# Performance work log

Hardware: AMD Instinct MI355X
Metric: run time of the kernel (lower is better)

Reference implementation:

```python
import jax, jax.numpy as jnp
import numpy as np

N_NODES = 100000
N_EDGES = 1600000
IN_CH = 165


def setup_inputs() -> dict:
    key = jax.random.key(0)
    ks = jax.random.split(key, 6)
    x = jax.random.normal(ks[0], (N_NODES, IN_CH), dtype=jnp.float32)
    edge_index = jax.random.randint(ks[1], (2, N_EDGES), 0, N_NODES, dtype=jnp.int32)
    # Glorot-ish init for weights
    W1 = jax.random.normal(ks[2], (IN_CH, 128), dtype=jnp.float32) * (1.0 / np.sqrt(IN_CH))
    b1 = jnp.zeros((128,), dtype=jnp.float32)
    W2 = jax.random.normal(ks[3], (128, 64), dtype=jnp.float32) * (1.0 / np.sqrt(128))
    b2 = jnp.zeros((64,), dtype=jnp.float32)
    Wo = jax.random.normal(ks[4], (64, 2), dtype=jnp.float32) * (1.0 / np.sqrt(64))
    bo = jnp.zeros((2,), dtype=jnp.float32)
    return {"x": x, "edge_index": edge_index, "W1": W1, "b1": b1,
            "W2": W2, "b2": b2, "Wo": Wo, "bo": bo}


def _gcn_norm(edge_index, n_nodes, dtype):
    """Add self-loops and compute symmetric normalization deg^-1/2 * deg^-1/2 (PyG gcn_norm)."""
    loops = jnp.arange(n_nodes, dtype=edge_index.dtype)
    ei = jnp.concatenate([edge_index, jnp.stack([loops, loops])], axis=1)
    row, col = ei[0], ei[1]
    deg = jax.ops.segment_sum(jnp.ones(ei.shape[1], dtype), col, num_segments=n_nodes)
    deg_inv_sqrt = jnp.where(deg > 0, jax.lax.rsqrt(deg), 0.0)
    norm = deg_inv_sqrt[row] * deg_inv_sqrt[col]  # [E+N]
    return row, col, norm


def _gcn_conv(h, row, col, norm, W, b, n_nodes):
    # transform first (F_in -> F_out), then gather-scale-scatter aggregate
    m = h @ W                                   # [N, F_out]
    msg = m[row] * norm[:, None]                # [E+N, F_out]
    agg = jax.ops.segment_sum(msg, col, num_segments=n_nodes)
    return agg + b


def reference(x, edge_index, W1, b1, W2, b2, Wo, bo):
    n_nodes = x.shape[0]
    row, col, norm = _gcn_norm(edge_index, n_nodes, x.dtype)
    h = jax.nn.relu(_gcn_conv(x, row, col, norm, W1, b1, n_nodes))
    h = jax.nn.relu(_gcn_conv(h, row, col, norm, W2, b2, n_nodes))
    return h @ Wo + bo  # [N, 2] logits
```

## Files before the change

kernel.cpp:

```cpp
#include <hip/hip_runtime.h>

#define N_NODES 100000
#define N_EDGES 1600000
#define IN_CH   165
#define SCAN_CHUNK 2048
#define NB_SCAN ((N_NODES + SCAN_CHUNK - 1) / SCAN_CHUNK)
#define BSHIFT 7
#define NBUCK  ((N_NODES + 127) / 128)
#define BCAP   3072
#define PA_BLOCKS 196

typedef unsigned short ushort_t;
typedef _Float16 f16;
typedef _Float16 f16x2 __attribute__((ext_vector_type(2)));
typedef _Float16 f16x8 __attribute__((ext_vector_type(8)));
typedef _Float16 hfrag8 __attribute__((ext_vector_type(8)));
typedef short bfrag8 __attribute__((ext_vector_type(8)));
typedef float f32x4 __attribute__((ext_vector_type(4)));

__device__ __forceinline__ ushort_t f2bf(float f) {
    unsigned u = __float_as_uint(f);
    unsigned r = (u + 0x7fffu + ((u >> 16) & 1u)) >> 16;
    return (ushort_t)r;
}
__device__ __forceinline__ float bf2f(ushort_t h) {
    return __uint_as_float(((unsigned)h) << 16);
}

__device__ __forceinline__ void fmix_lo(float& a, unsigned pair) {
    asm("v_fma_mix_f32 %0, %1, 1.0, %0 op_sel_hi:[1,0,0]" : "+v"(a) : "v"(pair));
}
__device__ __forceinline__ void fmix_hi(float& a, unsigned pair) {
    asm("v_fma_mix_f32 %0, %1, 1.0, %0 op_sel:[1,0,0] op_sel_hi:[1,0,0]" : "+v"(a) : "v"(pair));
}
__device__ __forceinline__ void fmix_acc8(float* acc, uint4 v) {
    fmix_lo(acc[0], v.x); fmix_hi(acc[1], v.x);
    fmix_lo(acc[2], v.y); fmix_hi(acc[3], v.y);
    fmix_lo(acc[4], v.z); fmix_hi(acc[5], v.z);
    fmix_lo(acc[6], v.w); fmix_hi(acc[7], v.w);
}

__global__ void scan1_kernel(const int* __restrict__ cnt, int* __restrict__ off,
                             int* __restrict__ bsum, int n) {
    __shared__ int sh[256];
    int t = threadIdx.x;
    int base = blockIdx.x * SCAN_CHUNK + t * 8;
    int v[8];
    int run = 0;
    #pragma unroll
    for (int j = 0; j < 8; ++j) {
        int c = (base + j < n) ? cnt[base + j] : 0;
        v[j] = run; run += c;
    }
    sh[t] = run;
    __syncthreads();
    for (int o = 1; o < 256; o <<= 1) {
        int x = (t >= o) ? sh[t - o] : 0;
        __syncthreads();
        sh[t] += x;
        __syncthreads();
    }
    int prev = (t > 0) ? sh[t - 1] : 0;
    #pragma unroll
    for (int j = 0; j < 8; ++j)
        if (base + j < n) off[base + j] = prev + v[j];
    if (t == 255) bsum[blockIdx.x] = sh[255];
}

__global__ void scan2_kernel(int* bsum, int nb) {
    int lane = threadIdx.x;
    int orig = (lane < nb) ? bsum[lane] : 0;
    int v = orig;
    #pragma unroll
    for (int o = 1; o < 64; o <<= 1) {
        int t = __shfl_up(v, o);
        if (lane >= o) v += t;
    }
    if (lane < nb) bsum[lane] = v - orig;
}

__global__ void scan3_kernel(int* __restrict__ off, const int* __restrict__ bsum,
                             int n, int E) {
    int i = blockIdx.x * blockDim.x + threadIdx.x;
    if (i < n) {
        off[i] = off[i] + bsum[i / SCAN_CHUNK];
    } else if (i == n) {
        off[n] = E;
    }
}

__global__ void bucketA_kernel(const int* __restrict__ row, const int* __restrict__ col,
                               int* __restrict__ bfill, unsigned* __restrict__ tmp) {
    __shared__ int lcnt[NBUCK];
    __shared__ int lcur[NBUCK];
    int t = threadIdx.x;
    int e0 = (int)((long)blockIdx.x * N_EDGES / PA_BLOCKS);
    int e1 = (int)((long)(blockIdx.x + 1) * N_EDGES / PA_BLOCKS);
    for (int i = t; i < NBUCK; i += 256) lcnt[i] = 0;
    __syncthreads();
    for (int e = e0 + t; e < e1; e += 256)
        atomicAdd(&lcnt[col[e] >> BSHIFT], 1);
    __syncthreads();
    for (int b = t; b < NBUCK; b += 256) {
        int c = lcnt[b];
        lcur[b] = (c > 0) ? (b * BCAP + atomicAdd(&bfill[b], c)) : 0;
    }
    __syncthreads();
    for (int e = e0 + t; e < e1; e += 256) {
        int cc = col[e];
        int b = cc >> BSHIFT;
        int p = atomicAdd(&lcur[b], 1);
        tmp[p] = ((unsigned)(cc & 127) << 17) | (unsigned)row[e];
    }
}

__global__ void countB_kernel(const unsigned* __restrict__ tmp, const int* __restrict__ bfill,
                              int* __restrict__ cnt, float* __restrict__ dis) {
    __shared__ int lcnt[128];
    int b = blockIdx.x, t = threadIdx.x;
    if (t < 128) lcnt[t] = 0;
    __syncthreads();
    int total = min(bfill[b], BCAP);
    const unsigned* reg = tmp + (size_t)b * BCAP;
    for (int i = t; i < total; i += 256)
        atomicAdd(&lcnt[(reg[i] >> 17) & 127], 1);
    __syncthreads();
    if (t < 128) {
        int n = (b << BSHIFT) + t;
        if (n < N_NODES) {
            int c = lcnt[t];
            cnt[n] = c;
            dis[n] = rsqrtf((float)(c + 1));
        }
    }
}

__global__ void bucketB_kernel(const unsigned* __restrict__ tmp, const int* __restrict__ bfill,
                               const int* __restrict__ off, int* __restrict__ srt) {
    __shared__ int lcur[128];
    int b = blockIdx.x;
    int t = threadIdx.x;
    int nb0 = b << BSHIFT;
    int hi = min(nb0 + 128, N_NODES);
    int base = off[nb0];
    if (t < 128) {
        int nn = nb0 + t;
        lcur[t] = (nn < hi) ? off[nn] - base : 0;
    }
    __syncthreads();
    int total = min(bfill[b], BCAP);
    const unsigned* reg = tmp + (size_t)b * BCAP;
    for (int i = t; i < total; i += 256) {
        unsigned e = reg[i];
        int c = (e >> 17) & 127;
        int r = (int)(e & 0x1FFFFu);
        int p = atomicAdd(&lcur[c], 1);
        srt[base + p] = r;
    }
}

__global__ void wsplit_kernel(const float* __restrict__ W1, const float* __restrict__ W2,
                              ushort_t* __restrict__ wt1h, ushort_t* __restrict__ wt1l,
                              ushort_t* __restrict__ wt2h, ushort_t* __restrict__ wt2l) {
    int i = blockIdx.x * 256 + threadIdx.x;
    if (i < 128 * 192) {
        int ch = i / 192, k = i - ch * 192;
        float v = (k < IN_CH) ? W1[(size_t)k * 128 + ch] : 0.f;
        ushort_t h = f2bf(v);
        wt1h[i] = h;
        wt1l[i] = f2bf(v - bf2f(h));
    } else if (i < 128 * 192 + 64 * 128) {
        int j = i - 128 * 192;
        int ch = j / 128, k = j - ch * 128;
        float v = W2[(size_t)k * 64 + ch];
        f16 h = (f16)v;
        f16 l = (f16)(v - (float)h);
        wt2h[j] = *(ushort_t*)&h;
        wt2l[j] = *(ushort_t*)&l;
    }
}

__launch_bounds__(256)
__global__ void mfma_gemm1_kernel(const float* __restrict__ X,
                                  const ushort_t* __restrict__ wth,
                                  const ushort_t* __restrict__ wtl,
                                  const float* __restrict__ dis,
                                  f16* __restrict__ M, int n_nodes) {
    constexpr int NOUT = 128, KTOT = 165, KPAD = 192;
    constexpr int NCT = NOUT / 16;
    constexpr int NCHUNK = KPAD / 32;
    constexpr int XP = 40;
    constexpr int NW = 2;
    __shared__ ushort_t xsh[64][XP];
    __shared__ ushort_t xsl[64][XP];
    __shared__ ushort_t wsh[NOUT][XP];
    __shared__ ushort_t wsl[NOUT][XP];

    int t = threadIdx.x;
    int l = t & 63, wid = t >> 6;
    long node0 = (long)blockIdx.x * 64;

    int arow = wid * 16 + (l & 15);
    int kq = (l >> 4) * 8;

    f32x4 acc[NCT];
    #pragma unroll
    for (int ct = 0; ct < NCT; ++ct) acc[ct] = (f32x4){0.f, 0.f, 0.f, 0.f};

    float xa[4], xb[4];
    bfrag8 wfh[NW], wfl[NW];

    auto loadX = [&](int c) {
        int k0 = c * 32;
        #pragma unroll
        for (int i = 0; i < 4; ++i) {
            int idx = t + i * 256;
            int node = idx >> 4, kp = idx & 15;
            long g = node0 + node;
            int k = k0 + 2 * kp;
            bool ok = (g < n_nodes);
            xa[i] = (ok && k < KTOT) ? X[g * KTOT + k] : 0.f;
            xb[i] = (ok && k + 1 < KTOT) ? X[g * KTOT + k + 1] : 0.f;
        }
    };
    auto loadW = [&](int c) {
        int k0 = c * 32;
        #pragma unroll
        for (int i = 0; i < NW; ++i) {
            int idx = t + i * 256;
            int ch = idx >> 2, q = idx & 3;
            wfh[i] = *(const bfrag8*)&wth[(size_t)ch * KPAD + k0 + q * 8];
            wfl[i] = *(const bfrag8*)&wtl[(size_t)ch * KPAD + k0 + q * 8];
        }
    };
    auto storeLDS = [&]() {
        #pragma unroll
        for (int i = 0; i < 4; ++i) {
            int idx = t + i * 256;
            int node = idx >> 4, kp = idx & 15;
            ushort_t ha = (ushort_t)(__float_as_uint(xa[i]) >> 16);
            ushort_t la = f2bf(xa[i] - bf2f(ha));
            ushort_t hb = (ushort_t)(__float_as_uint(xb[i]) >> 16);
            ushort_t lb = f2bf(xb[i] - bf2f(hb));
            *(unsigned*)&xsh[node][2 * kp] = (unsigned)ha | ((unsigned)hb << 16);
            *(unsigned*)&xsl[node][2 * kp] = (unsigned)la | ((unsigned)lb << 16);
        }
        #pragma unroll
        for (int i = 0; i < NW; ++i) {
            int idx = t + i * 256;
            int ch = idx >> 2, q = idx & 3;
            *(bfrag8*)&wsh[ch][q * 8] = wfh[i];
            *(bfrag8*)&wsl[ch][q * 8] = wfl[i];
        }
    };

    loadX(0); loadW(0);
    for (int c = 0; c < NCHUNK; ++c) {
        storeLDS();
        __syncthreads();
        if (c + 1 < NCHUNK) { loadX(c + 1); loadW(c + 1); }
        bfrag8 ah = *(const bfrag8*)&xsh[arow][kq];
        bfrag8 al = *(const bfrag8*)&xsl[arow][kq];
        #pragma unroll
        for (int ct = 0; ct < NCT; ++ct) {
            bfrag8 bh = *(const bfrag8*)&wsh[ct * 16 + (l & 15)][kq];
            bfrag8 bl = *(const bfrag8*)&wsl[ct * 16 + (l & 15)][kq];
            acc[ct] = __builtin_amdgcn_mfma_f32_16x16x32_bf16(ah, bh, acc[ct], 0, 0, 0);
            acc[ct] = __builtin_amdgcn_mfma_f32_16x16x32_bf16(ah, bl, acc[ct], 0, 0, 0);
            acc[ct] = __builtin_amdgcn_mfma_f32_16x16x32_bf16(al, bh, acc[ct], 0, 0, 0);
        }
        __syncthreads();
    }

    int nl = wid * 16 + (l >> 4) * 4;
    float dv[4];
    #pragma unroll
    for (int j = 0; j < 4; ++j) {
        long node = node0 + nl + j;
        dv[j] = (node < n_nodes) ? dis[node] : 0.f;
    }
    #pragma unroll
    for (int ct = 0; ct < NCT; ++ct) {
        int ch = ct * 16 + (l & 15);
        #pragma unroll
        for (int j = 0; j < 4; ++j) {
            long node = node0 + nl + j;
            if (node < n_nodes)
                M[node * NOUT + ch] = (f16)(acc[ct][j] * dv[j]);
        }
    }
}

__launch_bounds__(256)
__global__ void mfma_gemm2_kernel(const f16* __restrict__ X,
                                  const ushort_t* __restrict__ wth,
                                  const ushort_t* __restrict__ wtl,
                                  const float* __restrict__ dis,
                                  f16* __restrict__ M, int n_nodes) {
    constexpr int NOUT = 64, KTOT = 128;
    constexpr int NCT = NOUT / 16;
    constexpr int NCHUNK = KTOT / 32;
    constexpr int XP = 40;
    __shared__ ushort_t xs[64][XP];
    __shared__ ushort_t wsh[NOUT][XP];
    __shared__ ushort_t wsl[NOUT][XP];

    int t = threadIdx.x;
    int l = t & 63, wid = t >> 6;
    long node0 = (long)blockIdx.x * 64;

    int arow = wid * 16 + (l & 15);
    int kq = (l >> 4) * 8;

    f32x4 acc[NCT];
    #pragma unroll
    for (int ct = 0; ct < NCT; ++ct) acc[ct] = (f32x4){0.f, 0.f, 0.f, 0.f};

    unsigned xu[4];
    bfrag8 wfh, wfl;

    auto loadX = [&](int c) {
        int k0 = c * 32;
        #pragma unroll
        for (int i = 0; i < 4; ++i) {
            int idx = t + i * 256;
            int node = idx >> 4, kp = idx & 15;
            long g = node0 + node;
            xu[i] = (g < n_nodes) ? *(const unsigned*)&X[g * KTOT + k0 + 2 * kp] : 0u;
        }
    };
    auto loadW = [&](int c) {
        int k0 = c * 32;
        int ch = t >> 2, q = t & 3;
        wfh = *(const bfrag8*)&wth[(size_t)ch * KTOT + k0 + q * 8];
        wfl = *(const bfrag8*)&wtl[(size_t)ch * KTOT + k0 + q * 8];
    };
    auto storeLDS = [&]() {
        #pragma unroll
        for (int i = 0; i < 4; ++i) {
            int idx = t + i * 256;
            int node = idx >> 4, kp = idx & 15;
            *(unsigned*)&xs[node][2 * kp] = xu[i];
        }
        int ch = t >> 2, q = t & 3;
        *(bfrag8*)&wsh[ch][q * 8] = wfh;
        *(bfrag8*)&wsl[ch][q * 8] = wfl;
    };

    loadX(0); loadW(0);
    for (int c = 0; c < NCHUNK; ++c) {
        storeLDS();
        __syncthreads();
        if (c + 1 < NCHUNK) { loadX(c + 1); loadW(c + 1); }
        hfrag8 a = *(const hfrag8*)&xs[arow][kq];
        #pragma unroll
        for (int ct = 0; ct < NCT; ++ct) {
            hfrag8 bh = *(const hfrag8*)&wsh[ct * 16 + (l & 15)][kq];
            hfrag8 bl = *(const hfrag8*)&wsl[ct * 16 + (l & 15)][kq];
            acc[ct] = __builtin_amdgcn_mfma_f32_16x16x32_f16(a, bh, acc[ct], 0, 0, 0);
            acc[ct] = __builtin_amdgcn_mfma_f32_16x16x32_f16(a, bl, acc[ct], 0, 0, 0);
        }
        __syncthreads();
    }

    int nl = wid * 16 + (l >> 4) * 4;
    float dv[4];
    #pragma unroll
    for (int j = 0; j < 4; ++j) {
        long node = node0 + nl + j;
        dv[j] = (node < n_nodes) ? dis[node] : 0.f;
    }
    #pragma unroll
    for (int ct = 0; ct < NCT; ++ct) {
        int ch = ct * 16 + (l & 15);
        #pragma unroll
        for (int j = 0; j < 4; ++j) {
            long node = node0 + nl + j;
            if (node < n_nodes)
                M[node * NOUT + ch] = (f16)(acc[ct][j] * dv[j]);
        }
    }
}

__global__ void agg1_kernel(const f16* __restrict__ ms, const int* __restrict__ srt,
                            const int* __restrict__ off, const float* __restrict__ dis,
                            const float* __restrict__ b1, f16* __restrict__ h1) {
    int wave = threadIdx.x >> 6;
    int lane = threadIdx.x & 63;
    int n = blockIdx.x * 4 + wave;
    if (n >= N_NODES) return;
    int g = lane >> 4, p = lane & 15;
    const char* msb = (const char*)ms;
    unsigned pb = (unsigned)p * 16;
    float dn = dis[n];
    float acc[8] = {0.f, 0.f, 0.f, 0.f, 0.f, 0.f, 0.f, 0.f};
    if (g == 0) {
        uint4 v = *(const uint4*)(msb + (unsigned)n * 256 + pb);
        fmix_acc8(acc, v);
    }
    int s0 = off[n], s1 = off[n + 1];
    int sv = (s0 + lane < s1) ? srt[s0 + lane] : 0;
    for (int base = s0; base < s1; base += 64) {
        int nb2 = base + 64;
        int svn = (nb2 + lane < s1) ? srt[nb2 + lane] : 0;
        int cnt = min(64, s1 - base);
        int j = 0;
        for (; j + 15 < cnt; j += 16) {
            unsigned o0 = (unsigned)__shfl(sv, j + g) * 256 + pb;
            unsigned o1 = (unsigned)__shfl(sv, j + 4 + g) * 256 + pb;
            unsigned o2 = (unsigned)__shfl(sv, j + 8 + g) * 256 + pb;
            unsigned o3 = (unsigned)__shfl(sv, j + 12 + g) * 256 + pb;
            uint4 v0 = *(const uint4*)(msb + o0);
            uint4 v1 = *(const uint4*)(msb + o1);
            uint4 v2 = *(const uint4*)(msb + o2);
            uint4 v3 = *(const uint4*)(msb + o3);
            fmix_acc8(acc, v0);
            fmix_acc8(acc, v1);
            fmix_acc8(acc, v2);
            fmix_acc8(acc, v3);
        }
        for (; j < cnt; j += 4) {
            int idx = __shfl(sv, j + g);
            float wm = (j + g < cnt) ? 1.f : 0.f;
            f16x8 v = *(const f16x8*)(msb + (unsigned)idx * 256 + pb);
            #pragma unroll
            for (int i = 0; i < 8; ++i) acc[i] = fmaf(wm, (float)v[i], acc[i]);
        }
        sv = svn;
    }
    #pragma unroll
    for (int i = 0; i < 8; ++i) {
        acc[i] += __shfl_xor(acc[i], 16);
        acc[i] += __shfl_xor(acc[i], 32);
    }
    if (lane < 16) {
        float4 ba = ((const float4*)b1)[lane * 2];
        float4 bb = ((const float4*)b1)[lane * 2 + 1];
        float bv[8] = {ba.x, ba.y, ba.z, ba.w, bb.x, bb.y, bb.z, bb.w};
        f16x8 r;
        #pragma unroll
        for (int i = 0; i < 8; ++i)
            r[i] = (f16)fmaxf(acc[i] * dn + bv[i], 0.f);
        *(f16x8*)(h1 + (size_t)n * 128 + lane * 8) = r;
    }
}

__global__ void agg2_kernel(const f16* __restrict__ ms, const int* __restrict__ srt,
                            const int* __restrict__ off, const float* __restrict__ dis,
                            const float* __restrict__ b2, const float* __restrict__ Wo,
                            const float* __restrict__ bo, float* __restrict__ out) {
    int wave = threadIdx.x >> 6;
    int lane = threadIdx.x & 63;
    int n = blockIdx.x * 4 + wave;
    if (n >= N_NODES) return;
    int g = lane >> 3, p = lane & 7;
    const char* msb = (const char*)ms;
    unsigned pb = (unsigned)p * 16;
    float dn = dis[n];
    float acc[8] = {0.f, 0.f, 0.f, 0.f, 0.f, 0.f, 0.f, 0.f};
    if (g == 0) {
        uint4 v = *(const uint4*)(msb + (unsigned)n * 128 + pb);
        fmix_acc8(acc, v);
    }
    int s0 = off[n], s1 = off[n + 1];
    int sv = (s0 + lane < s1) ? srt[s0 + lane] : 0;
    for (int base = s0; base < s1; base += 64) {
        int nb2 = base + 64;
        int svn = (nb2 + lane < s1) ? srt[nb2 + lane] : 0;
        int cnt = min(64, s1 - base);
        int j = 0;
        for (; j + 15 < cnt; j += 16) {
            unsigned o0 = (unsigned)__shfl(sv, j + g) * 128 + pb;
            unsigned o1 = (unsigned)__shfl(sv, j + 8 + g) * 128 + pb;
            uint4 v0 = *(const uint4*)(msb + o0);
            uint4 v1 = *(const uint4*)(msb + o1);
            fmix_acc8(acc, v0);
            fmix_acc8(acc, v1);
        }
        for (; j < cnt; j += 8) {
            int idx = __shfl(sv, j + g);
            float wm = (j + g < cnt) ? 1.f : 0.f;
            f16x8 v = *(const f16x8*)(msb + (unsigned)idx * 128 + pb);
            #pragma unroll
            for (int i = 0; i < 8; ++i) acc[i] = fmaf(wm, (float)v[i], acc[i]);
        }
        sv = svn;
    }
    #pragma unroll
    for (int i = 0; i < 8; ++i) {
        acc[i] += __shfl_xor(acc[i], 8);
        acc[i] += __shfl_xor(acc[i], 16);
        acc[i] += __shfl_xor(acc[i], 32);
    }
    float p0 = 0.f, p1 = 0.f;
    #pragma unroll
    for (int i = 0; i < 8; ++i) {
        int ch = p * 8 + i;
        float hc = fmaxf(acc[i] * dn + b2[ch], 0.f);
        p0 = fmaf(hc, Wo[ch * 2], p0);
        p1 = fmaf(hc, Wo[ch * 2 + 1], p1);
    }
    p0 += __shfl_xor(p0, 1); p1 += __shfl_xor(p1, 1);
    p0 += __shfl_xor(p0, 2); p1 += __shfl_xor(p1, 2);
    p0 += __shfl_xor(p0, 4); p1 += __shfl_xor(p1, 4);
    if (lane == 0) {
        out[(size_t)n * 2]     = p0 + bo[0];
        out[(size_t)n * 2 + 1] = p1 + bo[1];
    }
}

extern "C" void kernel_launch(void* const* d_in, const int* in_sizes, int n_in,
                              void* d_out, int out_size, void* d_ws, size_t ws_size,
                              hipStream_t stream) {
    const float* x  = (const float*)d_in[0];
    const int*   ei = (const int*)d_in[1];
    const int*   row = ei;
    const int*   col = ei + N_EDGES;
    const float* W1 = (const float*)d_in[2];
    const float* b1 = (const float*)d_in[3];
    const float* W2 = (const float*)d_in[4];
    const float* b2 = (const float*)d_in[5];
    const float* Wo = (const float*)d_in[6];
    const float* bo = (const float*)d_in[7];
    float* out = (float*)d_out;

    char* base = (char*)d_ws;
    auto alloc = [&](size_t bytes) {
        char* p = base;
        base += (bytes + 255) & ~(size_t)255;
        return p;
    };
    int*      cnt  = (int*)alloc((size_t)N_NODES * 4);
    int*      off  = (int*)alloc((size_t)(N_NODES + 1) * 4);
    float*    dis  = (float*)alloc((size_t)N_NODES * 4);
    int*      bsum = (int*)alloc(256);
    int*      bfill= (int*)alloc((size_t)NBUCK * 4);
    unsigned* tmp  = (unsigned*)alloc((size_t)NBUCK * BCAP * 4 + 4096);
    int*      srt  = (int*)alloc((size_t)N_EDGES * 4);
    f16*      m    = (f16*)alloc((size_t)N_NODES * 128 * 2);
    f16*      h1   = (f16*)alloc((size_t)N_NODES * 128 * 2);
    ushort_t* wt1h = (ushort_t*)alloc((size_t)128 * 192 * 2);
    ushort_t* wt1l = (ushort_t*)alloc((size_t)128 * 192 * 2);
    ushort_t* wt2h = (ushort_t*)alloc((size_t)64 * 128 * 2);
    ushort_t* wt2l = (ushort_t*)alloc((size_t)64 * 128 * 2);

    hipMemsetAsync(bfill, 0, (size_t)NBUCK * 4, stream);
    bucketA_kernel<<<PA_BLOCKS, 256, 0, stream>>>(row, col, bfill, tmp);
    countB_kernel<<<NBUCK, 256, 0, stream>>>(tmp, bfill, cnt, dis);
    scan1_kernel<<<NB_SCAN, 256, 0, stream>>>(cnt, off, bsum, N_NODES);
    scan2_kernel<<<1, 64, 0, stream>>>(bsum, NB_SCAN);
    scan3_kernel<<<(N_NODES + 256) / 256, 256, 0, stream>>>(off, bsum, N_NODES, N_EDGES);
    bucketB_kernel<<<NBUCK, 256, 0, stream>>>(tmp, bfill, off, srt);
    wsplit_kernel<<<(128 * 192 + 64 * 128 + 255) / 256, 256, 0, stream>>>(W1, W2, wt1h, wt1l, wt2h, wt2l);

    mfma_gemm1_kernel<<<(N_NODES + 63) / 64, 256, 0, stream>>>(x, wt1h, wt1l, dis, m, N_NODES);
    agg1_kernel<<<(N_NODES + 3) / 4, 256, 0, stream>>>(m, srt, off, dis, b1, h1);

    mfma_gemm2_kernel<<<(N_NODES + 63) / 64, 256, 0, stream>>>(h1, wt2h, wt2l, dis, m, N_NODES);
    agg2_kernel<<<(N_NODES + 3) / 4, 256, 0, stream>>>(m, srt, off, dis, b2, Wo, bo, out);
}
```

Before: 241.3 us.

## Fuse edge bucketing with first GEMM and move degree normalization into aggregation

Merges the edge bucketing pass and the first GEMM into one launch, with block ranges picking the role, so the two independent stages share the GPU. The three-kernel node-offset scan becomes a bucket-level scan plus a per-bucket local scan inside the sort kernel. The GEMMs no longer scale rows by deg^-1/2. Instead each sorted edge packs the source degree into its upper bits, and the aggregation kernels recompute rsqrt weights per edge through the fma_mix scale operand. This removes several launches and the dis array, in exchange for extra rsqrt work per gathered edge and a packed-bit format that limits node-index and degree ranges.

Measured after the change: 207.5 us. 1.16x faster.

```diff
diff --git a/kernel.cpp b/kernel.cpp
--- a/kernel.cpp
+++ b/kernel.cpp
@@ -3,8 +3,6 @@
 #define N_NODES 100000
 #define N_EDGES 1600000
 #define IN_CH   165
-#define SCAN_CHUNK 2048
-#define NB_SCAN ((N_NODES + SCAN_CHUNK - 1) / SCAN_CHUNK)
 #define BSHIFT 7
 #define NBUCK  ((N_NODES + 127) / 128)
 #define BCAP   3072
@@ -12,7 +10,6 @@
 
 typedef unsigned short ushort_t;
 typedef _Float16 f16;
-typedef _Float16 f16x2 __attribute__((ext_vector_type(2)));
 typedef _Float16 f16x8 __attribute__((ext_vector_type(8)));
 typedef _Float16 hfrag8 __attribute__((ext_vector_type(8)));
 typedef short bfrag8 __attribute__((ext_vector_type(8)));
@@ -27,136 +24,17 @@
     return __uint_as_float(((unsigned)h) << 16);
 }
 
-__device__ __forceinline__ void fmix_lo(float& a, unsigned pair) {
-    asm("v_fma_mix_f32 %0, %1, 1.0, %0 op_sel_hi:[1,0,0]" : "+v"(a) : "v"(pair));
-}
-__device__ __forceinline__ void fmix_hi(float& a, unsigned pair) {
-    asm("v_fma_mix_f32 %0, %1, 1.0, %0 op_sel:[1,0,0] op_sel_hi:[1,0,0]" : "+v"(a) : "v"(pair));
-}
-__device__ __forceinline__ void fmix_acc8(float* acc, uint4 v) {
-    fmix_lo(acc[0], v.x); fmix_hi(acc[1], v.x);
-    fmix_lo(acc[2], v.y); fmix_hi(acc[3], v.y);
-    fmix_lo(acc[4], v.z); fmix_hi(acc[5], v.z);
-    fmix_lo(acc[6], v.w); fmix_hi(acc[7], v.w);
-}
-
-__global__ void scan1_kernel(const int* __restrict__ cnt, int* __restrict__ off,
-                             int* __restrict__ bsum, int n) {
-    __shared__ int sh[256];
-    int t = threadIdx.x;
-    int base = blockIdx.x * SCAN_CHUNK + t * 8;
-    int v[8];
-    int run = 0;
-    #pragma unroll
-    for (int j = 0; j < 8; ++j) {
-        int c = (base + j < n) ? cnt[base + j] : 0;
-        v[j] = run; run += c;
-    }
-    sh[t] = run;
-    __syncthreads();
-    for (int o = 1; o < 256; o <<= 1) {
-        int x = (t >= o) ? sh[t - o] : 0;
-        __syncthreads();
-        sh[t] += x;
-        __syncthreads();
-    }
-    int prev = (t > 0) ? sh[t - 1] : 0;
-    #pragma unroll
-    for (int j = 0; j < 8; ++j)
-        if (base + j < n) off[base + j] = prev + v[j];
-    if (t == 255) bsum[blockIdx.x] = sh[255];
-}
-
-__global__ void scan2_kernel(int* bsum, int nb) {
-    int lane = threadIdx.x;
-    int orig = (lane < nb) ? bsum[lane] : 0;
-    int v = orig;
-    #pragma unroll
-    for (int o = 1; o < 64; o <<= 1) {
-        int t = __shfl_up(v, o);
-        if (lane >= o) v += t;
-    }
-    if (lane < nb) bsum[lane] = v - orig;
-}
-
-__global__ void scan3_kernel(int* __restrict__ off, const int* __restrict__ bsum,
-                             int n, int E) {
-    int i = blockIdx.x * blockDim.x + threadIdx.x;
-    if (i < n) {
-        off[i] = off[i] + bsum[i / SCAN_CHUNK];
-    } else if (i == n) {
-        off[n] = E;
-    }
-}
-
-__global__ void bucketA_kernel(const int* __restrict__ row, const int* __restrict__ col,
-                               int* __restrict__ bfill, unsigned* __restrict__ tmp) {
-    __shared__ int lcnt[NBUCK];
-    __shared__ int lcur[NBUCK];
-    int t = threadIdx.x;
-    int e0 = (int)((long)blockIdx.x * N_EDGES / PA_BLOCKS);
-    int e1 = (int)((long)(blockIdx.x + 1) * N_EDGES / PA_BLOCKS);
-    for (int i = t; i < NBUCK; i += 256) lcnt[i] = 0;
-    __syncthreads();
-    for (int e = e0 + t; e < e1; e += 256)
-        atomicAdd(&lcnt[col[e] >> BSHIFT], 1);
-    __syncthreads();
-    for (int b = t; b < NBUCK; b += 256) {
-        int c = lcnt[b];
-        lcur[b] = (c > 0) ? (b * BCAP + atomicAdd(&bfill[b], c)) : 0;
-    }
-    __syncthreads();
-    for (int e = e0 + t; e < e1; e += 256) {
-        int cc = col[e];
-        int b = cc >> BSHIFT;
-        int p = atomicAdd(&lcur[b], 1);
-        tmp[p] = ((unsigned)(cc & 127) << 17) | (unsigned)row[e];
-    }
-}
-
-__global__ void countB_kernel(const unsigned* __restrict__ tmp, const int* __restrict__ bfill,
-                              int* __restrict__ cnt, float* __restrict__ dis) {
-    __shared__ int lcnt[128];
-    int b = blockIdx.x, t = threadIdx.x;
-    if (t < 128) lcnt[t] = 0;
-    __syncthreads();
-    int total = min(bfill[b], BCAP);
-    const unsigned* reg = tmp + (size_t)b * BCAP;
-    for (int i = t; i < total; i += 256)
-        atomicAdd(&lcnt[(reg[i] >> 17) & 127], 1);
-    __syncthreads();
-    if (t < 128) {
-        int n = (b << BSHIFT) + t;
-        if (n < N_NODES) {
-            int c = lcnt[t];
-            cnt[n] = c;
-            dis[n] = rsqrtf((float)(c + 1));
-        }
-    }
-}
-
-__global__ void bucketB_kernel(const unsigned* __restrict__ tmp, const int* __restrict__ bfill,
-                               const int* __restrict__ off, int* __restrict__ srt) {
-    __shared__ int lcur[128];
-    int b = blockIdx.x;
-    int t = threadIdx.x;
-    int nb0 = b << BSHIFT;
-    int hi = min(nb0 + 128, N_NODES);
-    int base = off[nb0];
-    if (t < 128) {
-        int nn = nb0 + t;
-        lcur[t] = (nn < hi) ? off[nn] - base : 0;
-    }
-    __syncthreads();
-    int total = min(bfill[b], BCAP);
-    const unsigned* reg = tmp + (size_t)b * BCAP;
-    for (int i = t; i < total; i += 256) {
-        unsigned e = reg[i];
-        int c = (e >> 17) & 127;
-        int r = (int)(e & 0x1FFFFu);
-        int p = atomicAdd(&lcur[c], 1);
-        srt[base + p] = r;
-    }
+__device__ __forceinline__ void fmix_lo(float& a, unsigned pair, float s) {
+    asm("v_fma_mix_f32 %0, %1, %2, %0 op_sel_hi:[1,0,0]" : "+v"(a) : "v"(pair), "v"(s));
+}
+__device__ __forceinline__ void fmix_hi(float& a, unsigned pair, float s) {
+    asm("v_fma_mix_f32 %0, %1, %2, %0 op_sel:[1,0,0] op_sel_hi:[1,0,0]" : "+v"(a) : "v"(pair), "v"(s));
+}
+__device__ __forceinline__ void fmix_acc8(float* acc, uint4 v, float s) {
+    fmix_lo(acc[0], v.x, s); fmix_hi(acc[1], v.x, s);
+    fmix_lo(acc[2], v.y, s); fmix_hi(acc[3], v.y, s);
+    fmix_lo(acc[4], v.z, s); fmix_hi(acc[5], v.z, s);
+    fmix_lo(acc[6], v.w, s); fmix_hi(acc[7], v.w, s);
 }
 
 __global__ void wsplit_kernel(const float* __restrict__ W1, const float* __restrict__ W2,
@@ -181,113 +59,208 @@
 }
 
 __launch_bounds__(256)
-__global__ void mfma_gemm1_kernel(const float* __restrict__ X,
-                                  const ushort_t* __restrict__ wth,
-                                  const ushort_t* __restrict__ wtl,
-                                  const float* __restrict__ dis,
-                                  f16* __restrict__ M, int n_nodes) {
-    constexpr int NOUT = 128, KTOT = 165, KPAD = 192;
-    constexpr int NCT = NOUT / 16;
-    constexpr int NCHUNK = KPAD / 32;
-    constexpr int XP = 40;
-    constexpr int NW = 2;
-    __shared__ ushort_t xsh[64][XP];
-    __shared__ ushort_t xsl[64][XP];
-    __shared__ ushort_t wsh[NOUT][XP];
-    __shared__ ushort_t wsl[NOUT][XP];
-
+__global__ void l1_kernel(const int* __restrict__ row, const int* __restrict__ col,
+                          int* __restrict__ bfill, unsigned* __restrict__ tmp,
+                          const float* __restrict__ X,
+                          const ushort_t* __restrict__ wth, const ushort_t* __restrict__ wtl,
+                          f16* __restrict__ M, int n_nodes) {
+    __shared__ char smem[30720];
     int t = threadIdx.x;
-    int l = t & 63, wid = t >> 6;
-    long node0 = (long)blockIdx.x * 64;
-
-    int arow = wid * 16 + (l & 15);
-    int kq = (l >> 4) * 8;
-
-    f32x4 acc[NCT];
-    #pragma unroll
-    for (int ct = 0; ct < NCT; ++ct) acc[ct] = (f32x4){0.f, 0.f, 0.f, 0.f};
-
-    float xa[4], xb[4];
-    bfrag8 wfh[NW], wfl[NW];
-
-    auto loadX = [&](int c) {
-        int k0 = c * 32;
-        #pragma unroll
-        for (int i = 0; i < 4; ++i) {
-            int idx = t + i * 256;
-            int node = idx >> 4, kp = idx & 15;
-            long g = node0 + node;
-            int k = k0 + 2 * kp;
-            bool ok = (g < n_nodes);
-            xa[i] = (ok && k < KTOT) ? X[g * KTOT + k] : 0.f;
-            xb[i] = (ok && k + 1 < KTOT) ? X[g * KTOT + k + 1] : 0.f;
-        }
-    };
-    auto loadW = [&](int c) {
-        int k0 = c * 32;
-        #pragma unroll
-        for (int i = 0; i < NW; ++i) {
-            int idx = t + i * 256;
-            int ch = idx >> 2, q = idx & 3;
-            wfh[i] = *(const bfrag8*)&wth[(size_t)ch * KPAD + k0 + q * 8];
-            wfl[i] = *(const bfrag8*)&wtl[(size_t)ch * KPAD + k0 + q * 8];
-        }
-    };
-    auto storeLDS = [&]() {
-        #pragma unroll
-        for (int i = 0; i < 4; ++i) {
-            int idx = t + i * 256;
-            int node = idx >> 4, kp = idx & 15;
-            ushort_t ha = (ushort_t)(__float_as_uint(xa[i]) >> 16);
-            ushort_t la = f2bf(xa[i] - bf2f(ha));
-            ushort_t hb = (ushort_t)(__float_as_uint(xb[i]) >> 16);
-            ushort_t lb = f2bf(xb[i] - bf2f(hb));
-            *(unsigned*)&xsh[node][2 * kp] = (unsigned)ha | ((unsigned)hb << 16);
-            *(unsigned*)&xsl[node][2 * kp] = (unsigned)la | ((unsigned)lb << 16);
-        }
-        #pragma unroll
-        for (int i = 0; i < NW; ++i) {
-            int idx = t + i * 256;
-            int ch = idx >> 2, q = idx & 3;
-            *(bfrag8*)&wsh[ch][q * 8] = wfh[i];
-            *(bfrag8*)&wsl[ch][q * 8] = wfl[i];
-        }
-    };
-
-    loadX(0); loadW(0);
-    for (int c = 0; c < NCHUNK; ++c) {
-        storeLDS();
-        __syncthreads();
-        if (c + 1 < NCHUNK) { loadX(c + 1); loadW(c + 1); }
-        bfrag8 ah = *(const bfrag8*)&xsh[arow][kq];
-        bfrag8 al = *(const bfrag8*)&xsl[arow][kq];
+    if (blockIdx.x < PA_BLOCKS) {
+        int* lcnt = (int*)smem;
+        int* lcur = ((int*)smem) + NBUCK;
+        int e0 = (int)((long)blockIdx.x * N_EDGES / PA_BLOCKS);
+        int e1 = (int)((long)(blockIdx.x + 1) * N_EDGES / PA_BLOCKS);
+        for (int i = t; i < NBUCK; i += 256) lcnt[i] = 0;
+        __syncthreads();
+        for (int e = e0 + t; e < e1; e += 256)
+            atomicAdd(&lcnt[col[e] >> BSHIFT], 1);
+        __syncthreads();
+        for (int b = t; b < NBUCK; b += 256) {
+            int c = lcnt[b];
+            lcur[b] = (c > 0) ? (b * BCAP + atomicAdd(&bfill[b], c)) : 0;
+        }
+        __syncthreads();
+        for (int e = e0 + t; e < e1; e += 256) {
+            int cc = col[e];
+            int b = cc >> BSHIFT;
+            int p = atomicAdd(&lcur[b], 1);
+            tmp[p] = ((unsigned)(cc & 127) << 17) | (unsigned)row[e];
+        }
+    } else {
+        constexpr int NOUT = 128, KTOT = 165, KPAD = 192;
+        constexpr int NCT = NOUT / 16;
+        constexpr int NCHUNK = KPAD / 32;
+        constexpr int XP = 40;
+        ushort_t (*xsh)[XP] = (ushort_t(*)[XP])(smem);
+        ushort_t (*xsl)[XP] = (ushort_t(*)[XP])(smem + 5120);
+        ushort_t (*wsh)[XP] = (ushort_t(*)[XP])(smem + 10240);
+        ushort_t (*wsl)[XP] = (ushort_t(*)[XP])(smem + 20480);
+
+        int l = t & 63, wid = t >> 6;
+        long node0 = (long)(blockIdx.x - PA_BLOCKS) * 64;
+        int arow = wid * 16 + (l & 15);
+        int kq = (l >> 4) * 8;
+
+        f32x4 acc[NCT];
+        #pragma unroll
+        for (int ct = 0; ct < NCT; ++ct) acc[ct] = (f32x4){0.f, 0.f, 0.f, 0.f};
+
+        float xa[4], xb[4];
+        bfrag8 wfh[2], wfl[2];
+
+        auto loadX = [&](int c) {
+            int k0 = c * 32;
+            #pragma unroll
+            for (int i = 0; i < 4; ++i) {
+                int idx = t + i * 256;
+                int node = idx >> 4, kp = idx & 15;
+                long g = node0 + node;
+                int k = k0 + 2 * kp;
+                bool ok = (g < n_nodes);
+                xa[i] = (ok && k < KTOT) ? X[g * KTOT + k] : 0.f;
+                xb[i] = (ok && k + 1 < KTOT) ? X[g * KTOT + k + 1] : 0.f;
+            }
+        };
+        auto loadW = [&](int c) {
+            int k0 = c * 32;
+            #pragma unroll
+            for (int i = 0; i < 2; ++i) {
+                int idx = t + i * 256;
+                int ch = idx >> 2, q = idx & 3;
+                wfh[i] = *(const bfrag8*)&wth[(size_t)ch * KPAD + k0 + q * 8];
+                wfl[i] = *(const bfrag8*)&wtl[(size_t)ch * KPAD + k0 + q * 8];
+            }
+        };
+        auto storeLDS = [&]() {
+            #pragma unroll
+            for (int i = 0; i < 4; ++i) {
+                int idx = t + i * 256;
+                int node = idx >> 4, kp = idx & 15;
+                ushort_t ha = (ushort_t)(__float_as_uint(xa[i]) >> 16);
+                ushort_t la = f2bf(xa[i] - bf2f(ha));
+                ushort_t hb = (ushort_t)(__float_as_uint(xb[i]) >> 16);
+                ushort_t lb = f2bf(xb[i] - bf2f(hb));
+                *(unsigned*)&xsh[node][2 * kp] = (unsigned)ha | ((unsigned)hb << 16);
+                *(unsigned*)&xsl[node][2 * kp] = (unsigned)la | ((unsigned)lb << 16);
+            }
+            #pragma unroll
+            for (int i = 0; i < 2; ++i) {
+                int idx = t + i * 256;
+                int ch = idx >> 2, q = idx & 3;
+                *(bfrag8*)&wsh[ch][q * 8] = wfh[i];
+                *(bfrag8*)&wsl[ch][q * 8] = wfl[i];
+            }
+        };
+
+        loadX(0); loadW(0);
+        for (int c = 0; c < NCHUNK; ++c) {
+            storeLDS();
+            __syncthreads();
+            if (c + 1 < NCHUNK) { loadX(c + 1); loadW(c + 1); }
+            bfrag8 ah = *(const bfrag8*)&xsh[arow][kq];
+            bfrag8 al = *(const bfrag8*)&xsl[arow][kq];
+            #pragma unroll
+            for (int ct = 0; ct < NCT; ++ct) {
+                bfrag8 bh = *(const bfrag8*)&wsh[ct * 16 + (l & 15)][kq];
+                bfrag8 bl = *(const bfrag8*)&wsl[ct * 16 + (l & 15)][kq];
+                acc[ct] = __builtin_amdgcn_mfma_f32_16x16x32_bf16(ah, bh, acc[ct], 0, 0, 0);
+                acc[ct] = __builtin_amdgcn_mfma_f32_16x16x32_bf16(ah, bl, acc[ct], 0, 0, 0);
+                acc[ct] = __builtin_amdgcn_mfma_f32_16x16x32_bf16(al, bh, acc[ct], 0, 0, 0);
+            }
+            __syncthreads();
+        }
+
+        int nl = wid * 16 + (l >> 4) * 4;
         #pragma unroll
         for (int ct = 0; ct < NCT; ++ct) {
-            bfrag8 bh = *(const bfrag8*)&wsh[ct * 16 + (l & 15)][kq];
-            bfrag8 bl = *(const bfrag8*)&wsl[ct * 16 + (l & 15)][kq];
-            acc[ct] = __builtin_amdgcn_mfma_f32_16x16x32_bf16(ah, bh, acc[ct], 0, 0, 0);
-            acc[ct] = __builtin_amdgcn_mfma_f32_16x16x32_bf16(ah, bl, acc[ct], 0, 0, 0);
-            acc[ct] = __builtin_amdgcn_mfma_f32_16x16x32_bf16(al, bh, acc[ct], 0, 0, 0);
-        }
-        __syncthreads();
-    }
-
-    int nl = wid * 16 + (l >> 4) * 4;
-    float dv[4];
-    #pragma unroll
-    for (int j = 0; j < 4; ++j) {
-        long node = node0 + nl + j;
-        dv[j] = (node < n_nodes) ? dis[node] : 0.f;
-    }
-    #pragma unroll
-    for (int ct = 0; ct < NCT; ++ct) {
-        int ch = ct * 16 + (l & 15);
+            int ch = ct * 16 + (l & 15);
+            #pragma unroll
+            for (int j = 0; j < 4; ++j) {
+                long node = node0 + nl + j;
+                if (node < n_nodes)
+                    M[node * NOUT + ch] = (f16)acc[ct][j];
+            }
+        }
+    }
+}
+
+__global__ void prep_kernel(const unsigned* __restrict__ tmp, const int* __restrict__ bfill,
+                            int* __restrict__ cnt, int* __restrict__ bbase,
+                            int* __restrict__ off) {
+    __shared__ int lcnt[128];
+    __shared__ int ssc[256];
+    int b = blockIdx.x, t = threadIdx.x;
+    if (t < 128) lcnt[t] = 0;
+    __syncthreads();
+    int total = min(bfill[b], BCAP);
+    const unsigned* reg = tmp + (size_t)b * BCAP;
+    for (int i = t; i < total; i += 256)
+        atomicAdd(&lcnt[(reg[i] >> 17) & 127], 1);
+    __syncthreads();
+    if (t < 128) {
+        int n = (b << BSHIFT) + t;
+        if (n < N_NODES) cnt[n] = lcnt[t];
+    }
+    if (b == 0) {
+        int v[4]; int run = 0;
+        int base = t * 4;
         #pragma unroll
         for (int j = 0; j < 4; ++j) {
-            long node = node0 + nl + j;
-            if (node < n_nodes)
-                M[node * NOUT + ch] = (f16)(acc[ct][j] * dv[j]);
-        }
+            int c = (base + j < NBUCK) ? bfill[base + j] : 0;
+            v[j] = run; run += c;
+        }
+        ssc[t] = run;
+        __syncthreads();
+        for (int o = 1; o < 256; o <<= 1) {
+            int x = (t >= o) ? ssc[t - o] : 0;
+            __syncthreads();
+            ssc[t] += x;
+            __syncthreads();
+        }
+        int prev = (t > 0) ? ssc[t - 1] : 0;
+        #pragma unroll
+        for (int j = 0; j < 4; ++j)
+            if (base + j < NBUCK) bbase[base + j] = prev + v[j];
+        if (t == 0) off[N_NODES] = N_EDGES;
+    }
+}
+
+__global__ void bucketB2_kernel(const unsigned* __restrict__ tmp, const int* __restrict__ bfill,
+                                const int* __restrict__ bbase, const int* __restrict__ cnt,
+                                int* __restrict__ off, unsigned* __restrict__ srt) {
+    __shared__ int sh[128];
+    __shared__ int lcur[128];
+    int b = blockIdx.x, t = threadIdx.x;
+    int nb0 = b << BSHIFT;
+    int base = bbase[b];
+    if (t < 128) {
+        int n = nb0 + t;
+        sh[t] = (n < N_NODES) ? cnt[n] : 0;
+    }
+    __syncthreads();
+    for (int o = 1; o < 128; o <<= 1) {
+        int x = (t < 128 && t >= o) ? sh[t - o] : 0;
+        __syncthreads();
+        if (t < 128) sh[t] += x;
+        __syncthreads();
+    }
+    if (t < 128) {
+        int excl = (t > 0) ? sh[t - 1] : 0;
+        int n = nb0 + t;
+        if (n < N_NODES) off[n] = base + excl;
+        lcur[t] = excl;
+    }
+    __syncthreads();
+    int total = min(bfill[b], BCAP);
+    const unsigned* reg = tmp + (size_t)b * BCAP;
+    for (int i = t; i < total; i += 256) {
+        unsigned e = reg[i];
+        int c = (e >> 17) & 127;
+        unsigned src = e & 0x1FFFFu;
+        unsigned cs = min((unsigned)cnt[src], 255u);
+        int p = atomicAdd(&lcur[c], 1);
+        srt[base + p] = (cs << 17) | src;
     }
 }
 
@@ -295,7 +268,6 @@
 __global__ void mfma_gemm2_kernel(const f16* __restrict__ X,
                                   const ushort_t* __restrict__ wth,
                                   const ushort_t* __restrict__ wtl,
-                                  const float* __restrict__ dis,
                                   f16* __restrict__ M, int n_nodes) {
     constexpr int NOUT = 64, KTOT = 128;
     constexpr int NCT = NOUT / 16;
@@ -364,12 +336,6 @@
     }
 
     int nl = wid * 16 + (l >> 4) * 4;
-    float dv[4];
-    #pragma unroll
-    for (int j = 0; j < 4; ++j) {
-        long node = node0 + nl + j;
-        dv[j] = (node < n_nodes) ? dis[node] : 0.f;
-    }
     #pragma unroll
     for (int ct = 0; ct < NCT; ++ct) {
         int ch = ct * 16 + (l & 15);
@@ -377,13 +343,13 @@
         for (int j = 0; j < 4; ++j) {
             long node = node0 + nl + j;
             if (node < n_nodes)
-                M[node * NOUT + ch] = (f16)(acc[ct][j] * dv[j]);
-        }
-    }
-}
-
-__global__ void agg1_kernel(const f16* __restrict__ ms, const int* __restrict__ srt,
-                            const int* __restrict__ off, const float* __restrict__ dis,
+                M[node * NOUT + ch] = (f16)acc[ct][j];
+        }
+    }
+}
+
+__global__ void agg1_kernel(const f16* __restrict__ ms, const unsigned* __restrict__ srt,
+                            const int* __restrict__ off,
                             const float* __restrict__ b1, f16* __restrict__ h1) {
     int wave = threadIdx.x >> 6;
     int lane = threadIdx.x & 63;
@@ -392,39 +358,42 @@
     int g = lane >> 4, p = lane & 15;
     const char* msb = (const char*)ms;
     unsigned pb = (unsigned)p * 16;
-    float dn = dis[n];
+    int s0 = off[n], s1 = off[n + 1];
+    float dn = rsqrtf((float)(s1 - s0) + 1.f);
     float acc[8] = {0.f, 0.f, 0.f, 0.f, 0.f, 0.f, 0.f, 0.f};
     if (g == 0) {
         uint4 v = *(const uint4*)(msb + (unsigned)n * 256 + pb);
-        fmix_acc8(acc, v);
-    }
-    int s0 = off[n], s1 = off[n + 1];
-    int sv = (s0 + lane < s1) ? srt[s0 + lane] : 0;
+        fmix_acc8(acc, v, dn);
+    }
+    unsigned sv = (s0 + lane < s1) ? srt[s0 + lane] : 0;
     for (int base = s0; base < s1; base += 64) {
         int nb2 = base + 64;
-        int svn = (nb2 + lane < s1) ? srt[nb2 + lane] : 0;
-        int cnt = min(64, s1 - base);
+        unsigned svn = (nb2 + lane < s1) ? srt[nb2 + lane] : 0;
+        int cnt_ = min(64, s1 - base);
         int j = 0;
-        for (; j + 15 < cnt; j += 16) {
-            unsigned o0 = (unsigned)__shfl(sv, j + g) * 256 + pb;
-            unsigned o1 = (unsigned)__shfl(sv, j + 4 + g) * 256 + pb;
-            unsigned o2 = (unsigned)__shfl(sv, j + 8 + g) * 256 + pb;
-            unsigned o3 = (unsigned)__shfl(sv, j + 12 + g) * 256 + pb;
-            uint4 v0 = *(const uint4*)(msb + o0);
-            uint4 v1 = *(const uint4*)(msb + o1);
-            uint4 v2 = *(const uint4*)(msb + o2);
-            uint4 v3 = *(const uint4*)(msb + o3);
-            fmix_acc8(acc, v0);
-            fmix_acc8(acc, v1);
-            fmix_acc8(acc, v2);
-            fmix_acc8(acc, v3);
-        }
-        for (; j < cnt; j += 4) {
-            int idx = __shfl(sv, j + g);
-            float wm = (j + g < cnt) ? 1.f : 0.f;
-            f16x8 v = *(const f16x8*)(msb + (unsigned)idx * 256 + pb);
-            #pragma unroll
-            for (int i = 0; i < 8; ++i) acc[i] = fmaf(wm, (float)v[i], acc[i]);
+        for (; j + 15 < cnt_; j += 16) {
+            unsigned e0 = (unsigned)__shfl((int)sv, j + g);
+            unsigned e1 = (unsigned)__shfl((int)sv, j + 4 + g);
+            unsigned e2 = (unsigned)__shfl((int)sv, j + 8 + g);
+            unsigned e3 = (unsigned)__shfl((int)sv, j + 12 + g);
+            uint4 v0 = *(const uint4*)(msb + (e0 & 0x1FFFFu) * 256 + pb);
+            uint4 v1 = *(const uint4*)(msb + (e1 & 0x1FFFFu) * 256 + pb);
+            uint4 v2 = *(const uint4*)(msb + (e2 & 0x1FFFFu) * 256 + pb);
+            uint4 v3 = *(const uint4*)(msb + (e3 & 0x1FFFFu) * 256 + pb);
+            float d0 = rsqrtf((float)(e0 >> 17) + 1.f);
+            float d1 = rsqrtf((float)(e1 >> 17) + 1.f);
+            float d2 = rsqrtf((float)(e2 >> 17) + 1.f);
+            float d3 = rsqrtf((float)(e3 >> 17) + 1.f);
+            fmix_acc8(acc, v0, d0);
+            fmix_acc8(acc, v1, d1);
+            fmix_acc8(acc, v2, d2);
+            fmix_acc8(acc, v3, d3);
+        }
+        for (; j < cnt_; j += 4) {
+            unsigned e = (unsigned)__shfl((int)sv, j + g);
+            float ws = (j + g < cnt_) ? rsqrtf((float)(e >> 17) + 1.f) : 0.f;
+            uint4 v = *(const uint4*)(msb + (e & 0x1FFFFu) * 256 + pb);
+            fmix_acc8(acc, v, ws);
         }
         sv = svn;
     }
@@ -445,8 +414,8 @@
     }
 }
 
-__global__ void agg2_kernel(const f16* __restrict__ ms, const int* __restrict__ srt,
-                            const int* __restrict__ off, const float* __restrict__ dis,
+__global__ void agg2_kernel(const f16* __restrict__ ms, const unsigned* __restrict__ srt,
+                            const int* __restrict__ off,
                             const float* __restrict__ b2, const float* __restrict__ Wo,
                             const float* __restrict__ bo, float* __restrict__ out) {
     int wave = threadIdx.x >> 6;
@@ -456,33 +425,34 @@
     int g = lane >> 3, p = lane & 7;
     const char* msb = (const char*)ms;
     unsigned pb = (unsigned)p * 16;
-    float dn = dis[n];
+    int s0 = off[n], s1 = off[n + 1];
+    float dn = rsqrtf((float)(s1 - s0) + 1.f);
     float acc[8] = {0.f, 0.f, 0.f, 0.f, 0.f, 0.f, 0.f, 0.f};
     if (g == 0) {
         uint4 v = *(const uint4*)(msb + (unsigned)n * 128 + pb);
-        fmix_acc8(acc, v);
-    }
-    int s0 = off[n], s1 = off[n + 1];
-    int sv = (s0 + lane < s1) ? srt[s0 + lane] : 0;
+        fmix_acc8(acc, v, dn);
+    }
+    unsigned sv = (s0 + lane < s1) ? srt[s0 + lane] : 0;
     for (int base = s0; base < s1; base += 64) {
         int nb2 = base + 64;
-        int svn = (nb2 + lane < s1) ? srt[nb2 + lane] : 0;
-        int cnt = min(64, s1 - base);
+        unsigned svn = (nb2 + lane < s1) ? srt[nb2 + lane] : 0;
+        int cnt_ = min(64, s1 - base);
         int j = 0;
-        for (; j + 15 < cnt; j += 16) {
-            unsigned o0 = (unsigned)__shfl(sv, j + g) * 128 + pb;
-            unsigned o1 = (unsigned)__shfl(sv, j + 8 + g) * 128 + pb;
-            uint4 v0 = *(const uint4*)(msb + o0);
-            uint4 v1 = *(const uint4*)(msb + o1);
-            fmix_acc8(acc, v0);
-            fmix_acc8(acc, v1);
-        }
-        for (; j < cnt; j += 8) {
-            int idx = __shfl(sv, j + g);
-            float wm = (j + g < cnt) ? 1.f : 0.f;
-            f16x8 v = *(const f16x8*)(msb + (unsigned)idx * 128 + pb);
-            #pragma unroll
-            for (int i = 0; i < 8; ++i) acc[i] = fmaf(wm, (float)v[i], acc[i]);
+        for (; j + 15 < cnt_; j += 16) {
+            unsigned e0 = (unsigned)__shfl((int)sv, j + g);
+            unsigned e1 = (unsigned)__shfl((int)sv, j + 8 + g);
+            uint4 v0 = *(const uint4*)(msb + (e0 & 0x1FFFFu) * 128 + pb);
+            uint4 v1 = *(const uint4*)(msb + (e1 & 0x1FFFFu) * 128 + pb);
+            float d0 = rsqrtf((float)(e0 >> 17) + 1.f);
+            float d1 = rsqrtf((float)(e1 >> 17) + 1.f);
+            fmix_acc8(acc, v0, d0);
+            fmix_acc8(acc, v1, d1);
+        }
+        for (; j < cnt_; j += 8) {
+            unsigned e = (unsigned)__shfl((int)sv, j + g);
+            float ws = (j + g < cnt_) ? rsqrtf((float)(e >> 17) + 1.f) : 0.f;
+            uint4 v = *(const uint4*)(msb + (e & 0x1FFFFu) * 128 + pb);
+            fmix_acc8(acc, v, ws);
         }
         sv = svn;
     }
@@ -532,11 +502,10 @@
     };
     int*      cnt  = (int*)alloc((size_t)N_NODES * 4);
     int*      off  = (int*)alloc((size_t)(N_NODES + 1) * 4);
-    float*    dis  = (float*)alloc((size_t)N_NODES * 4);
-    int*      bsum = (int*)alloc(256);
+    int*      bbase= (int*)alloc((size_t)(NBUCK + 1) * 4);
     int*      bfill= (int*)alloc((size_t)NBUCK * 4);
     unsigned* tmp  = (unsigned*)alloc((size_t)NBUCK * BCAP * 4 + 4096);
-    int*      srt  = (int*)alloc((size_t)N_EDGES * 4);
+    unsigned* srt  = (unsigned*)alloc((size_t)N_EDGES * 4);
     f16*      m    = (f16*)alloc((size_t)N_NODES * 128 * 2);
     f16*      h1   = (f16*)alloc((size_t)N_NODES * 128 * 2);
     ushort_t* wt1h = (ushort_t*)alloc((size_t)128 * 192 * 2);
@@ -545,17 +514,16 @@
     ushort_t* wt2l = (ushort_t*)alloc((size_t)64 * 128 * 2);
 
     hipMemsetAsync(bfill, 0, (size_t)NBUCK * 4, stream);
-    bucketA_kernel<<<PA_BLOCKS, 256, 0, stream>>>(row, col, bfill, tmp);
-    countB_kernel<<<NBUCK, 256, 0, stream>>>(tmp, bfill, cnt, dis);
-    scan1_kernel<<<NB_SCAN, 256, 0, stream>>>(cnt, off, bsum, N_NODES);
-    scan2_kernel<<<1, 64, 0, stream>>>(bsum, NB_SCAN);
-    scan3_kernel<<<(N_NODES + 256) / 256, 256, 0, stream>>>(off, bsum, N_NODES, N_EDGES);
-    bucketB_kernel<<<NBUCK, 256, 0, stream>>>(tmp, bfill, off, srt);
     wsplit_kernel<<<(128 * 192 + 64 * 128 + 255) / 256, 256, 0, stream>>>(W1, W2, wt1h, wt1l, wt2h, wt2l);
 
-    mfma_gemm1_kernel<<<(N_NODES + 63) / 64, 256, 0, stream>>>(x, wt1h, wt1l, dis, m, N_NODES);
-    agg1_kernel<<<(N_NODES + 3) / 4, 256, 0, stream>>>(m, srt, off, dis, b1, h1);
-
-    mfma_gemm2_kernel<<<(N_NODES + 63) / 64, 256, 0, stream>>>(h1, wt2h, wt2l, dis, m, N_NODES);
-    agg2_kernel<<<(N_NODES + 3) / 4, 256, 0, stream>>>(m, srt, off, dis, b2, Wo, bo, out);
-}
+    int gemm1_blocks = (N_NODES + 63) / 64;
+    l1_kernel<<<PA_BLOCKS + gemm1_blocks, 256, 0, stream>>>(row, col, bfill, tmp,
+                                                            x, wt1h, wt1l, m, N_NODES);
+    prep_kernel<<<NBUCK, 256, 0, stream>>>(tmp, bfill, cnt, bbase, off);
+    bucketB2_kernel<<<NBUCK, 256, 0, stream>>>(tmp, bfill, bbase, cnt, off, srt);
+
+    agg1_kernel<<<(N_NODES + 3) / 4, 256, 0, stream>>>(m, srt, off, b1, h1);
+
+    mfma_gemm2_kernel<<<(N_NODES + 63) / 64, 256, 0, stream>>>(h1, wt2h, wt2l, m, N_NODES);
+    agg2_kernel<<<(N_NODES + 3) / 4, 256, 0, stream>>>(m, srt, off, b2, Wo, bo, out);
+}
```
